# Performance work log

Hardware: AMD Instinct MI355X
Metric: run time of the kernel (lower is better)

The kernel has to match this reference:

```python
import jax, jax.numpy as jnp
import numpy as np

GRID = (8192, 8192)   # 2D lattice, *dims
NDIM = 2              # links.shape[0]
P_LINK = 0.45         # subcritical bond probability -> finite clusters, bounded step count


def setup_inputs() -> dict:
    key = jax.random.key(0)
    k1, k2 = jax.random.split(key)
    # links[i] marks an open bond between site x and its +1 neighbour along axis i
    links = jax.random.uniform(k1, (NDIM,) + GRID) < P_LINK
    seed_idx = jax.random.randint(k2, (NDIM,), 0, GRID[0]).astype(jnp.int32)
    return {"links": links, "seed_idx": seed_idx}


def _flood_fill(links, seed_idx):
    """Faithful port of ClusterSelection.from_seed_idx: BFS-style roll+mask
    expansion iterated to fixed point via lax.while_loop."""
    ndim = links.shape[0]
    grid = links.shape[1:]
    selected0 = jnp.zeros(grid, dtype=bool).at[tuple(seed_idx)].set(True)

    def cond(carry):
        _, is_done, _ = carry
        return ~is_done

    def body(carry):
        sel0, _, steps = carry
        sel = sel0
        for i in range(ndim):  # unrolled over the (small, static) ndim
            # sites whose -1-neighbour or self is selected can use bond i
            links_to_try = sel0 | jnp.roll(sel0, -1, i)
            links_sel = links_to_try & links[i]
            # a taken bond marks both of its endpoints
            links_sel = links_sel | jnp.roll(links_sel, 1, i)
            sel = sel | links_sel
        is_done = (sel ^ sel0).sum() == 0
        return sel, is_done, steps + 1

    sel, _, steps = jax.lax.while_loop(
        cond, body, (selected0, jnp.array(False), jnp.array(0, jnp.int32))
    )
    return sel, steps


def reference(links, seed_idx):
    sel, _steps = _flood_fill(links, seed_idx)
    return sel
```

## Files before the change

### kernel.cpp

```cpp
#include <hip/hip_runtime.h>
#include <stdint.h>

#define GW 8192
#define GMASK 8191
#define PLANE 67108864ULL
#define TPD 128
#define TMASK 127
#define NTILES 16384
#define QCAP 65536
#define QMASK 65535
#define WPR 128

#define OFF_CTRL   0
#define OFF_TFLAGS 4096
#define OFF_QUEUE  8192
#define OFF_BITMAP 270336
#define CLEAR_BYTES 8658944

typedef unsigned long long u64;
typedef unsigned int u32;

__device__ __forceinline__ u64 aload64(const u64* p) {
    return __hip_atomic_load(p, __ATOMIC_RELAXED, __HIP_MEMORY_SCOPE_AGENT);
}
__device__ __forceinline__ int aload32(const int* p) {
    return __hip_atomic_load(p, __ATOMIC_ACQUIRE, __HIP_MEMORY_SCOPE_AGENT);
}

__global__ void clear_ws_kernel(uint4* __restrict__ p, int n) {
    int i = blockIdx.x * blockDim.x + threadIdx.x;
    if (i < n) p[i] = make_uint4(0, 0, 0, 0);
}

__global__ void init_kernel(const unsigned char* __restrict__ links8,
                            const int* __restrict__ seed_idx,
                            char* __restrict__ ws) {
    __shared__ int c1, c3;
    if (threadIdx.x == 0) { c1 = 0; c3 = 0; }
    __syncthreads();
    int l1 = 0, l3 = 0;
    for (int i = threadIdx.x; i < 16384; i += blockDim.x) {
        if (links8[i]) { int m = i & 3; if (m == 1) l1++; else if (m == 3) l3++; }
    }
    atomicAdd(&c1, l1);
    atomicAdd(&c3, l3);
    __syncthreads();
    if (threadIdx.x == 0) {
        int* ctrl = (int*)(ws + OFF_CTRL);
        u32* tflags = (u32*)(ws + OFF_TFLAGS);
        int* q = (int*)(ws + OFF_QUEUE);
        u64* bitmap = (u64*)(ws + OFF_BITMAP);
        ctrl[3] = (c1 > 0) ? 0 : ((c3 > 0) ? 2 : 1);
        int sr = seed_idx[0] & GMASK, sc = seed_idx[1] & GMASK;
        bitmap[(u64)sr * WPR + (sc >> 6)] = 1ull << (sc & 63);
        int t = (sr >> 6) * TPD + (sc >> 6);
        tflags[t >> 5] = 1u << (t & 31);
        q[0] = t + 1;
        ctrl[0] = 0;
        ctrl[1] = 1;
        ctrl[2] = 1;
    }
}

__device__ __forceinline__ u32 nib4(u32 w) {
    return (((w & 0x01010101u) * 0x01020408u) >> 24) & 0xFu;
}
__device__ __forceinline__ u64 pack_row_b8(const unsigned char* p) {
    const uint4* q = (const uint4*)p;
    u64 w = 0;
#pragma unroll
    for (int i = 0; i < 4; i++) {
        uint4 v = q[i];
        u64 nb = (u64)(nib4(v.x) | (nib4(v.y) << 4) | (nib4(v.z) << 8) | (nib4(v.w) << 12));
        w |= nb << (16 * i);
    }
    return w;
}
__device__ __forceinline__ u64 pack_row_b32(const u32* p) {
    u64 w = 0;
#pragma unroll
    for (int k = 0; k < 16; k++) {
        uint4 v = ((const uint4*)p)[k];
        u64 nb = (u64)((v.x != 0) | ((v.y != 0) << 1) | ((v.z != 0) << 2) | ((v.w != 0) << 3));
        w |= nb << (4 * k);
    }
    return w;
}

__global__ void __launch_bounds__(256)
bfs_tiles_kernel(const unsigned char* __restrict__ links8,
                 char* __restrict__ ws) {
    int* ctrl   = (int*)(ws + OFF_CTRL);
    u32* tflags = (u32*)(ws + OFF_TFLAGS);
    int* q      = (int*)(ws + OFF_QUEUE);
    u64* bitmap = (u64*)(ws + OFF_BITMAP);

    const int ln = threadIdx.x & 63;
    const int mode = ctrl[3];

    const unsigned char* p0b = links8;
    const unsigned char* p1b = links8 + PLANE;
    const u32* p0w = (const u32*)links8;
    const u32* p1w = (const u32*)(links8 + PLANE * 4);

    auto enq = [&](int t2) {
        u32 bit = 1u << (t2 & 31);
        __threadfence();
        u32 old = atomicOr(&tflags[t2 >> 5], bit);
        if (!(old & bit)) {
            atomicAdd(&ctrl[2], 1);
            int pos = atomicAdd(&ctrl[1], 1) & QMASK;
            __hip_atomic_store(&q[pos], t2 + 1, __ATOMIC_RELEASE, __HIP_MEMORY_SCOPE_AGENT);
        }
    };

    long long guard = 0;
    while (true) {
        int t = -1;
        if (ln == 0) {
            while (true) {
                if (aload32(&ctrl[2]) == 0) break;
                int h  = aload32(&ctrl[0]);
                int tl = aload32(&ctrl[1]);
                if (h != tl) {
                    if (atomicCAS((u32*)&ctrl[0], (u32)h, (u32)(h + 1)) == (u32)h) {
                        int pos = h & QMASK;
                        int v;
                        long long g2 = 0;
                        while ((v = __hip_atomic_load(&q[pos], __ATOMIC_ACQUIRE,
                                                      __HIP_MEMORY_SCOPE_AGENT)) == 0) {
                            __builtin_amdgcn_s_sleep(1);
                            if (++g2 > 10000000LL) break;
                        }
                        __hip_atomic_store(&q[pos], 0, __ATOMIC_RELEASE,
                                           __HIP_MEMORY_SCOPE_AGENT);
                        t = v - 1;
                        break;
                    }
                } else {
                    __builtin_amdgcn_s_sleep(8);
                }
                if (++guard > 200000000LL) break;
            }
        }
        t = __shfl(t, 0);
        if (t < 0) break;

        const int tR = t >> 7, tC = t & TMASK;
        if (ln == 0) atomicAnd(&tflags[t >> 5], ~(1u << (t & 31)));
        __threadfence();

        const int gr = tR * 64 + ln;
        u64* wp = &bitmap[(u64)gr * WPR + tC];
        u64 loaded = aload64(wp);

        u64 l0, l1;
        if (mode == 0) {
            l0 = pack_row_b8(p0b + (u64)gr * GW + tC * 64);
            l1 = pack_row_b8(p1b + (u64)gr * GW + tC * 64);
        } else {
            l0 = pack_row_b32(p0w + (u64)gr * GW + tC * 64);
            l1 = pack_row_b32(p1w + (u64)gr * GW + tC * 64);
        }

        u64 P0 = l1 & 0x7FFFFFFFFFFFFFFFull;
        u64 P1 = P0 & (P0 >> 1);
        u64 P2 = P1 & (P1 >> 2);
        u64 P3 = P2 & (P2 >> 4);
        u64 P4 = P3 & (P3 >> 8);
        u64 P5 = P4 & (P4 >> 16);
        u64 D0 = (ln < 63) ? l0 : 0ull;
        u64 D1 = D0 & __shfl_down(D0, 1);
        u64 D2 = D1 & __shfl_down(D1, 2);
        u64 D3 = D2 & __shfl_down(D2, 4);
        u64 D4 = D3 & __shfl_down(D3, 8);
        u64 D5 = D4 & __shfl_down(D4, 16);

        u64 sel = loaded;
        while (true) {
            u64 old = sel;
            sel |= (sel & P0) << 1;  sel |= (sel >> 1)  & P0;
            sel |= (sel & P1) << 2;  sel |= (sel >> 2)  & P1;
            sel |= (sel & P2) << 4;  sel |= (sel >> 4)  & P2;
            sel |= (sel & P3) << 8;  sel |= (sel >> 8)  & P3;
            sel |= (sel & P4) << 16; sel |= (sel >> 16) & P4;
            sel |= (sel & P5) << 32; sel |= (sel >> 32) & P5;
            sel |= __shfl_up(sel & D0, 1);  sel |= __shfl_down(sel, 1)  & D0;
            sel |= __shfl_up(sel & D1, 2);  sel |= __shfl_down(sel, 2)  & D1;
            sel |= __shfl_up(sel & D2, 4);  sel |= __shfl_down(sel, 4)  & D2;
            sel |= __shfl_up(sel & D3, 8);  sel |= __shfl_down(sel, 8)  & D3;
            sel |= __shfl_up(sel & D4, 16); sel |= __shfl_down(sel, 16) & D4;
            sel |= __shfl_up(sel & D5, 32); sel |= __shfl_down(sel, 32) & D5;
            if (__ballot(sel != old) == 0ull) break;
        }

        u64 newbits = sel & ~loaded;
        if (newbits) atomicOr(wp, newbits);

        const int c0 = tC * 64;
        bool rnew = false, lnew = false;
        if ((sel >> 63) & (l1 >> 63) & 1ull) {
            u64 old = atomicOr(&bitmap[(u64)gr * WPR + ((tC + 1) & TMASK)], 1ull);
            rnew = !(old & 1ull);
        }
        {
            u64 lcol = (u64)((c0 - 1) & GMASK);
            bool lopen = (mode == 0) ? (p1b[(u64)gr * GW + lcol] != 0)
                                     : (p1w[(u64)gr * GW + lcol] != 0);
            if ((sel & 1ull) && lopen) {
                u64 old = atomicOr(&bitmap[(u64)gr * WPR + ((tC - 1) & TMASK)], 1ull << 63);
                lnew = !(old & (1ull << 63));
            }
        }
        u64 rmask = __ballot(rnew), lmask = __ballot(lnew);

        const int ga = (tR * 64 - 1) & GMASK;
        bool bopen = (mode == 0) ? (p0b[(u64)ga * GW + c0 + ln] != 0)
                                 : (p0w[(u64)ga * GW + c0 + ln] != 0);
        u64 top_sel = __shfl(sel, 0);
        u64 umask = __ballot(bopen && ((top_sel >> ln) & 1));
        u64 unew = 0;
        if (ln == 0 && umask) {
            u64 old = atomicOr(&bitmap[(u64)ga * WPR + tC], umask);
            unew = umask & ~old;
        }
        u64 dmask = sel & l0;
        const int gb = (tR * 64 + 64) & GMASK;
        u64 dnew = 0;
        if (ln == 63 && dmask) {
            u64 old = atomicOr(&bitmap[(u64)gb * WPR + tC], dmask);
            dnew = dmask & ~old;
        }

        if (ln == 0  && rmask) enq(tR * TPD + ((tC + 1) & TMASK));
        if (ln == 1  && lmask) enq(tR * TPD + ((tC - 1) & TMASK));
        if (ln == 0  && unew)  enq(((tR - 1) & TMASK) * TPD + tC);
        if (ln == 63 && dnew)  enq(((tR + 1) & TMASK) * TPD + tC);

        __threadfence();
        if (ln == 0) atomicSub(&ctrl[2], 1);
    }
}

__global__ void writeout_kernel(const u64* __restrict__ bitmap, int4* __restrict__ out) {
    int g = blockIdx.x * blockDim.x + threadIdx.x;
    int site0 = g << 2;
    u64 w = bitmap[site0 >> 6];
    u32 b = (u32)(w >> (site0 & 63)) & 0xFu;
    out[g] = make_int4(b & 1, (b >> 1) & 1, (b >> 2) & 1, (b >> 3) & 1);
}

extern "C" void kernel_launch(void* const* d_in, const int* in_sizes, int n_in,
                              void* d_out, int out_size, void* d_ws, size_t ws_size,
                              hipStream_t stream) {
    const unsigned char* links = (const unsigned char*)d_in[0];
    const int* seed = (const int*)d_in[1];
    char* ws = (char*)d_ws;

    int n16 = CLEAR_BYTES / 16;
    clear_ws_kernel<<<(n16 + 255) / 256, 256, 0, stream>>>((uint4*)ws, n16);
    init_kernel<<<1, 256, 0, stream>>>(links, seed, ws);
    bfs_tiles_kernel<<<64, 256, 0, stream>>>(links, ws);
    writeout_kernel<<<65536, 256, 0, stream>>>((const u64*)(ws + OFF_BITMAP), (int4*)d_out);
}
```

Baseline: 705.3 us.

## Widen BFS tiles to 64x128 and add per-block LDS work queue

Tiles grow from 64x64 to 64x128, two bitmap words per row with a carry between the halves, which halves the tile count and the queue operations per area. Each block gets a shared-memory queue holding recently discovered neighbour tiles, and only overflow goes to the global atomic queue. The launch moves from 64 blocks of 256 threads to 32 blocks of 1024, so global queue contention and cross-block latency should drop. The cost is more register pressure per wave, possible load imbalance between blocks, and more complex termination handling.

```diff
diff --git a/kernel.cpp b/kernel.cpp
--- a/kernel.cpp
+++ b/kernel.cpp
@@ -4,12 +4,15 @@
 #define GW 8192
 #define GMASK 8191
 #define PLANE 67108864ULL
-#define TPD 128
-#define TMASK 127
-#define NTILES 16384
-#define QCAP 65536
-#define QMASK 65535
 #define WPR 128
+#define TR_CNT 128
+#define TC_CNT 64
+#define TRMASK 127
+#define TCMASK 63
+#define NTILES 8192
+#define OVF_MASK 65535
+#define LQ_CAP 4096
+#define LQ_MASK 4095
 
 #define OFF_CTRL   0
 #define OFF_TFLAGS 4096
@@ -20,9 +23,6 @@
 typedef unsigned long long u64;
 typedef unsigned int u32;
 
-__device__ __forceinline__ u64 aload64(const u64* p) {
-    return __hip_atomic_load(p, __ATOMIC_RELAXED, __HIP_MEMORY_SCOPE_AGENT);
-}
 __device__ __forceinline__ int aload32(const int* p) {
     return __hip_atomic_load(p, __ATOMIC_ACQUIRE, __HIP_MEMORY_SCOPE_AGENT);
 }
@@ -53,12 +53,10 @@
         ctrl[3] = (c1 > 0) ? 0 : ((c3 > 0) ? 2 : 1);
         int sr = seed_idx[0] & GMASK, sc = seed_idx[1] & GMASK;
         bitmap[(u64)sr * WPR + (sc >> 6)] = 1ull << (sc & 63);
-        int t = (sr >> 6) * TPD + (sc >> 6);
+        int t = (sr >> 6) * TC_CNT + (sc >> 7);
         tflags[t >> 5] = 1u << (t & 31);
         q[0] = t + 1;
-        ctrl[0] = 0;
-        ctrl[1] = 1;
-        ctrl[2] = 1;
+        ctrl[0] = 0; ctrl[1] = 1; ctrl[2] = 1;
     }
 }
 
@@ -87,21 +85,46 @@
     return w;
 }
 
-__global__ void __launch_bounds__(256)
+#define KS6(s, P0, P1, P2, P3, P4, P5)                         \
+    s |= (s & P0) << 1;  s |= (s >> 1)  & P0;                  \
+    s |= (s & P1) << 2;  s |= (s >> 2)  & P1;                  \
+    s |= (s & P2) << 4;  s |= (s >> 4)  & P2;                  \
+    s |= (s & P3) << 8;  s |= (s >> 8)  & P3;                  \
+    s |= (s & P4) << 16; s |= (s >> 16) & P4;                  \
+    s |= (s & P5) << 32; s |= (s >> 32) & P5;
+
+#define VS6(s, D0, D1, D2, D3, D4, D5)                                     \
+    s |= __shfl_up(s & D0, 1);  s |= __shfl_down(s, 1)  & D0;              \
+    s |= __shfl_up(s & D1, 2);  s |= __shfl_down(s, 2)  & D1;              \
+    s |= __shfl_up(s & D2, 4);  s |= __shfl_down(s, 4)  & D2;              \
+    s |= __shfl_up(s & D3, 8);  s |= __shfl_down(s, 8)  & D3;              \
+    s |= __shfl_up(s & D4, 16); s |= __shfl_down(s, 16) & D4;              \
+    s |= __shfl_up(s & D5, 32); s |= __shfl_down(s, 32) & D5;
+
+__global__ void __launch_bounds__(1024)
 bfs_tiles_kernel(const unsigned char* __restrict__ links8,
                  char* __restrict__ ws) {
     int* ctrl   = (int*)(ws + OFF_CTRL);
     u32* tflags = (u32*)(ws + OFF_TFLAGS);
-    int* q      = (int*)(ws + OFF_QUEUE);
+    int* ovq    = (int*)(ws + OFF_QUEUE);
     u64* bitmap = (u64*)(ws + OFF_BITMAP);
 
-    const int ln = threadIdx.x & 63;
-    const int mode = ctrl[3];
-
+    volatile __shared__ unsigned short lq[LQ_CAP];
+    __shared__ int s_lhead, s_ltail;
+
+    const int tid = threadIdx.x;
+    const int ln  = tid & 63;
+    const int wv  = tid >> 6;
+
+    for (int i = tid; i < LQ_CAP; i += 1024) lq[i] = 0xFFFF;
+    if (tid == 0) { s_lhead = 0; s_ltail = 0; }
+    __syncthreads();
+
+    const int mode = __hip_atomic_load(&ctrl[3], __ATOMIC_RELAXED, __HIP_MEMORY_SCOPE_AGENT);
     const unsigned char* p0b = links8;
     const unsigned char* p1b = links8 + PLANE;
     const u32* p0w = (const u32*)links8;
-    const u32* p1w = (const u32*)(links8 + PLANE * 4);
+    const u32* p1w = (const u32*)links8 + PLANE;
 
     auto enq = [&](int t2) {
         u32 bit = 1u << (t2 & 31);
@@ -109,8 +132,15 @@
         u32 old = atomicOr(&tflags[t2 >> 5], bit);
         if (!(old & bit)) {
             atomicAdd(&ctrl[2], 1);
-            int pos = atomicAdd(&ctrl[1], 1) & QMASK;
-            __hip_atomic_store(&q[pos], t2 + 1, __ATOMIC_RELEASE, __HIP_MEMORY_SCOPE_AGENT);
+            int pend = *(volatile int*)&s_ltail - *(volatile int*)&s_lhead;
+            if (pend < 12) {
+                int pos = atomicAdd(&s_ltail, 1) & LQ_MASK;
+                lq[pos] = (unsigned short)t2;
+            } else {
+                int pos = atomicAdd(&ctrl[1], 1) & OVF_MASK;
+                __hip_atomic_store(&ovq[pos], t2 + 1, __ATOMIC_RELEASE,
+                                   __HIP_MEMORY_SCOPE_AGENT);
+            }
         }
     };
 
@@ -119,123 +149,142 @@
         int t = -1;
         if (ln == 0) {
             while (true) {
-                if (aload32(&ctrl[2]) == 0) break;
-                int h  = aload32(&ctrl[0]);
-                int tl = aload32(&ctrl[1]);
+                int h = *(volatile int*)&s_lhead, tl = *(volatile int*)&s_ltail;
                 if (h != tl) {
-                    if (atomicCAS((u32*)&ctrl[0], (u32)h, (u32)(h + 1)) == (u32)h) {
-                        int pos = h & QMASK;
-                        int v;
-                        long long g2 = 0;
-                        while ((v = __hip_atomic_load(&q[pos], __ATOMIC_ACQUIRE,
-                                                      __HIP_MEMORY_SCOPE_AGENT)) == 0) {
+                    if (atomicCAS(&s_lhead, h, h + 1) == h) {
+                        int pos = h & LQ_MASK;
+                        unsigned short v; long long g2 = 0;
+                        while ((v = lq[pos]) == 0xFFFF) {
                             __builtin_amdgcn_s_sleep(1);
-                            if (++g2 > 10000000LL) break;
+                            if (++g2 > 4000000LL) break;
                         }
-                        __hip_atomic_store(&q[pos], 0, __ATOMIC_RELEASE,
-                                           __HIP_MEMORY_SCOPE_AGENT);
-                        t = v - 1;
-                        break;
+                        lq[pos] = 0xFFFF;
+                        t = v; break;
                     }
-                } else {
-                    __builtin_amdgcn_s_sleep(8);
+                    continue;
                 }
-                if (++guard > 200000000LL) break;
+                if (__hip_atomic_load(&ctrl[2], __ATOMIC_RELAXED,
+                                      __HIP_MEMORY_SCOPE_AGENT) == 0) break;
+                if (wv < 2) {
+                    int oh = aload32(&ctrl[0]), ot = aload32(&ctrl[1]);
+                    if (oh != ot) {
+                        if (atomicCAS((u32*)&ctrl[0], (u32)oh, (u32)(oh + 1)) == (u32)oh) {
+                            int pos = oh & OVF_MASK; int v; long long g2 = 0;
+                            while ((v = __hip_atomic_load(&ovq[pos], __ATOMIC_ACQUIRE,
+                                                          __HIP_MEMORY_SCOPE_AGENT)) == 0) {
+                                __builtin_amdgcn_s_sleep(1);
+                                if (++g2 > 10000000LL) break;
+                            }
+                            __hip_atomic_store(&ovq[pos], 0, __ATOMIC_RELEASE,
+                                               __HIP_MEMORY_SCOPE_AGENT);
+                            t = v - 1; break;
+                        }
+                        continue;
+                    }
+                }
+                __builtin_amdgcn_s_sleep(4);
+                if (++guard > 50000000LL) break;
             }
         }
         t = __shfl(t, 0);
         if (t < 0) break;
 
-        const int tR = t >> 7, tC = t & TMASK;
+        const int tR = t >> 6, tC = t & TCMASK;
         if (ln == 0) atomicAnd(&tflags[t >> 5], ~(1u << (t & 31)));
         __threadfence();
 
         const int gr = tR * 64 + ln;
-        u64* wp = &bitmap[(u64)gr * WPR + tC];
-        u64 loaded = aload64(wp);
-
-        u64 l0, l1;
+        const int c0 = tC * 128;
+        u64* wp = &bitmap[(u64)gr * WPR + tC * 2];
+        u64 ld0 = __hip_atomic_load(wp,     __ATOMIC_RELAXED, __HIP_MEMORY_SCOPE_AGENT);
+        u64 ld1 = __hip_atomic_load(wp + 1, __ATOMIC_RELAXED, __HIP_MEMORY_SCOPE_AGENT);
+
+        u64 l0a, l0b, l1a, l1b;
         if (mode == 0) {
-            l0 = pack_row_b8(p0b + (u64)gr * GW + tC * 64);
-            l1 = pack_row_b8(p1b + (u64)gr * GW + tC * 64);
+            const unsigned char* b0 = p0b + (u64)gr * GW + c0;
+            const unsigned char* b1 = p1b + (u64)gr * GW + c0;
+            l0a = pack_row_b8(b0); l0b = pack_row_b8(b0 + 64);
+            l1a = pack_row_b8(b1); l1b = pack_row_b8(b1 + 64);
         } else {
-            l0 = pack_row_b32(p0w + (u64)gr * GW + tC * 64);
-            l1 = pack_row_b32(p1w + (u64)gr * GW + tC * 64);
-        }
-
-        u64 P0 = l1 & 0x7FFFFFFFFFFFFFFFull;
-        u64 P1 = P0 & (P0 >> 1);
-        u64 P2 = P1 & (P1 >> 2);
-        u64 P3 = P2 & (P2 >> 4);
-        u64 P4 = P3 & (P3 >> 8);
-        u64 P5 = P4 & (P4 >> 16);
-        u64 D0 = (ln < 63) ? l0 : 0ull;
-        u64 D1 = D0 & __shfl_down(D0, 1);
-        u64 D2 = D1 & __shfl_down(D1, 2);
-        u64 D3 = D2 & __shfl_down(D2, 4);
-        u64 D4 = D3 & __shfl_down(D3, 8);
-        u64 D5 = D4 & __shfl_down(D4, 16);
-
-        u64 sel = loaded;
+            const u32* b0 = p0w + (u64)gr * GW + c0;
+            const u32* b1 = p1w + (u64)gr * GW + c0;
+            l0a = pack_row_b32(b0); l0b = pack_row_b32(b0 + 64);
+            l1a = pack_row_b32(b1); l1b = pack_row_b32(b1 + 64);
+        }
+
+        const u64 INNER = 0x7FFFFFFFFFFFFFFFull;
+        u64 Pa0 = l1a & INNER, Pa1 = Pa0 & (Pa0 >> 1), Pa2 = Pa1 & (Pa1 >> 2),
+            Pa3 = Pa2 & (Pa2 >> 4), Pa4 = Pa3 & (Pa3 >> 8), Pa5 = Pa4 & (Pa4 >> 16);
+        u64 Pb0 = l1b & INNER, Pb1 = Pb0 & (Pb0 >> 1), Pb2 = Pb1 & (Pb1 >> 2),
+            Pb3 = Pb2 & (Pb2 >> 4), Pb4 = Pb3 & (Pb3 >> 8), Pb5 = Pb4 & (Pb4 >> 16);
+        u64 Da0 = (ln < 63) ? l0a : 0ull;
+        u64 Da1 = Da0 & __shfl_down(Da0, 1), Da2 = Da1 & __shfl_down(Da1, 2),
+            Da3 = Da2 & __shfl_down(Da2, 4), Da4 = Da3 & __shfl_down(Da3, 8),
+            Da5 = Da4 & __shfl_down(Da4, 16);
+        u64 Db0 = (ln < 63) ? l0b : 0ull;
+        u64 Db1 = Db0 & __shfl_down(Db0, 1), Db2 = Db1 & __shfl_down(Db1, 2),
+            Db3 = Db2 & __shfl_down(Db2, 4), Db4 = Db3 & __shfl_down(Db3, 8),
+            Db5 = Db4 & __shfl_down(Db4, 16);
+        const u64 xb = (l1a >> 63) & 1ull;
+
+        u64 s0 = ld0, s1 = ld1;
         while (true) {
-            u64 old = sel;
-            sel |= (sel & P0) << 1;  sel |= (sel >> 1)  & P0;
-            sel |= (sel & P1) << 2;  sel |= (sel >> 2)  & P1;
-            sel |= (sel & P2) << 4;  sel |= (sel >> 4)  & P2;
-            sel |= (sel & P3) << 8;  sel |= (sel >> 8)  & P3;
-            sel |= (sel & P4) << 16; sel |= (sel >> 16) & P4;
-            sel |= (sel & P5) << 32; sel |= (sel >> 32) & P5;
-            sel |= __shfl_up(sel & D0, 1);  sel |= __shfl_down(sel, 1)  & D0;
-            sel |= __shfl_up(sel & D1, 2);  sel |= __shfl_down(sel, 2)  & D1;
-            sel |= __shfl_up(sel & D2, 4);  sel |= __shfl_down(sel, 4)  & D2;
-            sel |= __shfl_up(sel & D3, 8);  sel |= __shfl_down(sel, 8)  & D3;
-            sel |= __shfl_up(sel & D4, 16); sel |= __shfl_down(sel, 16) & D4;
-            sel |= __shfl_up(sel & D5, 32); sel |= __shfl_down(sel, 32) & D5;
-            if (__ballot(sel != old) == 0ull) break;
-        }
-
-        u64 newbits = sel & ~loaded;
-        if (newbits) atomicOr(wp, newbits);
-
-        const int c0 = tC * 64;
+            u64 o0 = s0, o1 = s1;
+            KS6(s0, Pa0, Pa1, Pa2, Pa3, Pa4, Pa5);
+            s1 |= (s0 >> 63) & xb;
+            KS6(s1, Pb0, Pb1, Pb2, Pb3, Pb4, Pb5);
+            s0 |= ((s1 & 1ull) & xb) << 63;
+            VS6(s0, Da0, Da1, Da2, Da3, Da4, Da5);
+            VS6(s1, Db0, Db1, Db2, Db3, Db4, Db5);
+            if (__ballot((s0 != o0) | (s1 != o1)) == 0ull) break;
+        }
+
+        u64 nb0 = s0 & ~ld0, nb1 = s1 & ~ld1;
+        if (nb0) atomicOr(wp, nb0);
+        if (nb1) atomicOr(wp + 1, nb1);
+
         bool rnew = false, lnew = false;
-        if ((sel >> 63) & (l1 >> 63) & 1ull) {
-            u64 old = atomicOr(&bitmap[(u64)gr * WPR + ((tC + 1) & TMASK)], 1ull);
+        if ((s1 >> 63) & (l1b >> 63) & 1ull) {
+            u64 old = atomicOr(&bitmap[(u64)gr * WPR + ((tC * 2 + 2) & (WPR - 1))], 1ull);
             rnew = !(old & 1ull);
         }
         {
-            u64 lcol = (u64)((c0 - 1) & GMASK);
+            int lcol = (c0 - 1) & GMASK;
             bool lopen = (mode == 0) ? (p1b[(u64)gr * GW + lcol] != 0)
                                      : (p1w[(u64)gr * GW + lcol] != 0);
-            if ((sel & 1ull) && lopen) {
-                u64 old = atomicOr(&bitmap[(u64)gr * WPR + ((tC - 1) & TMASK)], 1ull << 63);
+            if ((s0 & 1ull) && lopen) {
+                u64 old = atomicOr(&bitmap[(u64)gr * WPR + ((tC * 2 - 1) & (WPR - 1))],
+                                   1ull << 63);
                 lnew = !(old & (1ull << 63));
             }
         }
         u64 rmask = __ballot(rnew), lmask = __ballot(lnew);
 
         const int ga = (tR * 64 - 1) & GMASK;
-        bool bopen = (mode == 0) ? (p0b[(u64)ga * GW + c0 + ln] != 0)
-                                 : (p0w[(u64)ga * GW + c0 + ln] != 0);
-        u64 top_sel = __shfl(sel, 0);
-        u64 umask = __ballot(bopen && ((top_sel >> ln) & 1));
-        u64 unew = 0;
-        if (ln == 0 && umask) {
-            u64 old = atomicOr(&bitmap[(u64)ga * WPR + tC], umask);
-            unew = umask & ~old;
-        }
-        u64 dmask = sel & l0;
+        bool bo0 = (mode == 0) ? (p0b[(u64)ga * GW + c0 + ln] != 0)
+                               : (p0w[(u64)ga * GW + c0 + ln] != 0);
+        bool bo1 = (mode == 0) ? (p0b[(u64)ga * GW + c0 + 64 + ln] != 0)
+                               : (p0w[(u64)ga * GW + c0 + 64 + ln] != 0);
+        u64 ts0 = __shfl(s0, 0), ts1 = __shfl(s1, 0);
+        u64 um0 = __ballot(bo0 && ((ts0 >> ln) & 1));
+        u64 um1 = __ballot(bo1 && ((ts1 >> ln) & 1));
+        u64 un = 0;
+        if (ln == 0) {
+            if (um0) { u64 old = atomicOr(&bitmap[(u64)ga * WPR + tC * 2],     um0); un |= um0 & ~old; }
+            if (um1) { u64 old = atomicOr(&bitmap[(u64)ga * WPR + tC * 2 + 1], um1); un |= um1 & ~old; }
+        }
         const int gb = (tR * 64 + 64) & GMASK;
-        u64 dnew = 0;
-        if (ln == 63 && dmask) {
-            u64 old = atomicOr(&bitmap[(u64)gb * WPR + tC], dmask);
-            dnew = dmask & ~old;
-        }
-
-        if (ln == 0  && rmask) enq(tR * TPD + ((tC + 1) & TMASK));
-        if (ln == 1  && lmask) enq(tR * TPD + ((tC - 1) & TMASK));
-        if (ln == 0  && unew)  enq(((tR - 1) & TMASK) * TPD + tC);
-        if (ln == 63 && dnew)  enq(((tR + 1) & TMASK) * TPD + tC);
+        u64 dn = 0;
+        if (ln == 63) {
+            u64 dm0 = s0 & l0a, dm1 = s1 & l0b;
+            if (dm0) { u64 old = atomicOr(&bitmap[(u64)gb * WPR + tC * 2],     dm0); dn |= dm0 & ~old; }
+            if (dm1) { u64 old = atomicOr(&bitmap[(u64)gb * WPR + tC * 2 + 1], dm1); dn |= dm1 & ~old; }
+        }
+
+        if (ln == 0  && rmask) enq(tR * TC_CNT + ((tC + 1) & TCMASK));
+        if (ln == 1  && lmask) enq(tR * TC_CNT + ((tC - 1) & TCMASK));
+        if (ln == 0  && un)    enq(((tR - 1) & TRMASK) * TC_CNT + tC);
+        if (ln == 63 && dn)    enq(((tR + 1) & TRMASK) * TC_CNT + tC);
 
         __threadfence();
         if (ln == 0) atomicSub(&ctrl[2], 1);
@@ -260,6 +309,6 @@
     int n16 = CLEAR_BYTES / 16;
     clear_ws_kernel<<<(n16 + 255) / 256, 256, 0, stream>>>((uint4*)ws, n16);
     init_kernel<<<1, 256, 0, stream>>>(links, seed, ws);
-    bfs_tiles_kernel<<<64, 256, 0, stream>>>(links, ws);
+    bfs_tiles_kernel<<<32, 1024, 0, stream>>>(links, ws);
     writeout_kernel<<<65536, 256, 0, stream>>>((const u64*)(ws + OFF_BITMAP), (int4*)d_out);
 }
```

After: 696.2 us. Within noise of the previous version (-1.3%).
